# Optimization experiments

Measured on AMD Instinct MI355X. Metric: run time of the kernel, lower is better.

## Reference

```python
import jax, jax.numpy as jnp
import numpy as np

N = 50000          # nodes
E = 200000         # edges
IN_C = 16          # in_channels
HID_C = 32         # hidden_channels (NNConv output)
EDGE_D = 8         # edge_attr_dim
OUT_C = 32         # out_channels (gnn output)
MLP_H = 128        # q_head hidden_dim
N_ACT = 32         # num_actions


def setup_inputs() -> dict:
    key = jax.random.key(0)
    ks = jax.random.split(key, 16)
    s = 0.05
    inp = {
        "x": jax.random.normal(ks[0], (N, IN_C), jnp.float32),
        "edge_src": jax.random.randint(ks[1], (E,), 0, N, jnp.int32),
        "edge_dst": jax.random.randint(ks[2], (E,), 0, N, jnp.int32),
        "edge_attr": jax.random.normal(ks[3], (E, EDGE_D), jnp.float32),
        # edge_nn: Linear(EDGE_D, IN_C*HID_C) + ReLU
        "We": jax.random.normal(ks[4], (EDGE_D, IN_C * HID_C), jnp.float32) * s,
        "be": jnp.zeros((IN_C * HID_C,), jnp.float32),
        # NNConv root weight + bias
        "Wroot": jax.random.normal(ks[5], (IN_C, HID_C), jnp.float32) * s,
        "bconv": jnp.zeros((HID_C,), jnp.float32),
        # LayerNorm over hidden_channels
        "gamma": jnp.ones((HID_C,), jnp.float32),
        "beta": jnp.zeros((HID_C,), jnp.float32),
        # gnn.lin: Linear(HID_C, OUT_C)
        "Wlin": jax.random.normal(ks[6], (HID_C, OUT_C), jnp.float32) * s,
        "blin": jnp.zeros((OUT_C,), jnp.float32),
        # q_head: Linear(OUT_C, MLP_H) -> ReLU -> Linear(MLP_H, N_ACT)
        "Wq1": jax.random.normal(ks[7], (OUT_C, MLP_H), jnp.float32) * s,
        "bq1": jnp.zeros((MLP_H,), jnp.float32),
        "Wq2": jax.random.normal(ks[8], (MLP_H, N_ACT), jnp.float32) * s,
        "bq2": jnp.zeros((N_ACT,), jnp.float32),
    }
    return inp


def reference(x, edge_src, edge_dst, edge_attr,
              We, be, Wroot, bconv, gamma, beta,
              Wlin, blin, Wq1, bq1, Wq2, bq2):
    # --- NNConv: per-edge weight from edge MLP ---
    w_e = jax.nn.relu(edge_attr @ We + be)              # [E, IN_C*HID_C]
    w_e = w_e.reshape(E, IN_C, HID_C)
    x_j = x[edge_src]                                    # gather source feats [E, IN_C]
    msg = jnp.einsum('ei,eih->eh', x_j, w_e)             # per-edge matmul [E, HID_C]
    agg = jax.ops.segment_sum(msg, edge_dst, num_segments=N)  # scatter-add [N, HID_C]
    h = agg + x @ Wroot + bconv                          # root + bias
    # --- LayerNorm + ReLU + Linear ---
    mu = jnp.mean(h, axis=-1, keepdims=True)
    var = jnp.mean((h - mu) ** 2, axis=-1, keepdims=True)
    h = (h - mu) / jnp.sqrt(var + 1e-5) * gamma + beta
    h = jax.nn.relu(h)
    feat = h @ Wlin + blin                               # [N, OUT_C]
    # --- q_head MLP ---
    q = jax.nn.relu(feat @ Wq1 + bq1) @ Wq2 + bq2        # [N, N_ACT]
    return q.reshape(-1, N_ACT)
```

## Files before the change

kernel.cpp:

```cpp
#include <hip/hip_runtime.h>

#define NN   50000
#define NE   200000
#define INC  16
#define HIDC 32
#define EDGED 8
#define OUTC 32
#define MLPH 128
#define NACT 32

#define NPART 196

typedef float floatx4 __attribute__((ext_vector_type(4)));

__global__ __launch_bounds__(256) void hist_kernel(const int* __restrict__ edst,
                                                   int* __restrict__ deg) {
    int e = blockIdx.x * blockDim.x + threadIdx.x;
    if (e < NE) atomicAdd(&deg[edst[e]], 1);
}

__global__ __launch_bounds__(256) void partial_kernel(const int* __restrict__ deg,
                                                      int* __restrict__ partials) {
    __shared__ int sm[256];
    int t = threadIdx.x, i = blockIdx.x * 256 + t;
    sm[t] = (i < NN) ? deg[i] : 0;
    __syncthreads();
    #pragma unroll
    for (int off = 128; off > 0; off >>= 1) {
        if (t < off) sm[t] += sm[t + off];
        __syncthreads();
    }
    if (t == 0) partials[blockIdx.x] = sm[0];
}

__global__ __launch_bounds__(256) void scan_partials_kernel(const int* __restrict__ partials,
                                                            int* __restrict__ poff) {
    __shared__ int sm[256];
    int t = threadIdx.x;
    sm[t] = (t < NPART) ? partials[t] : 0;
    __syncthreads();
    for (int off = 1; off < 256; off <<= 1) {
        int v = (t >= off) ? sm[t - off] : 0;
        __syncthreads();
        sm[t] += v;
        __syncthreads();
    }
    poff[t] = (t == 0) ? 0 : sm[t - 1];
}

__global__ __launch_bounds__(256) void rowoff_kernel(const int* __restrict__ deg,
                                                     const int* __restrict__ poff,
                                                     int* __restrict__ row_off) {
    __shared__ int sm[256];
    int t = threadIdx.x, i = blockIdx.x * 256 + t;
    int d = (i < NN) ? deg[i] : 0;
    sm[t] = d;
    __syncthreads();
    for (int off = 1; off < 256; off <<= 1) {
        int v = (t >= off) ? sm[t - off] : 0;
        __syncthreads();
        sm[t] += v;
        __syncthreads();
    }
    int excl = sm[t] - d + poff[blockIdx.x];
    if (i < NN) {
        row_off[i] = excl;
        if (i == NN - 1) row_off[NN] = excl + d;
    }
}

__global__ __launch_bounds__(256) void build_pos_kernel(const int* __restrict__ edst,
                                                        const int* __restrict__ row_off,
                                                        int* __restrict__ cursor,
                                                        int* __restrict__ epos) {
    int e = blockIdx.x * blockDim.x + threadIdx.x;
    if (e < NE) {
        int dst = edst[e];
        epos[e] = row_off[dst] + atomicAdd(&cursor[dst], 1);
    }
}

__global__ __launch_bounds__(256, 2) void edge_q4_kernel(
    const float* __restrict__ x,
    const int*   __restrict__ esrc,
    const float* __restrict__ ea,
    const float* __restrict__ We,
    const float* __restrict__ be,
    const int*   __restrict__ epos,
    float*       __restrict__ sorted_msg)
{
    __shared__ float sWe2[4 * 1032];
    __shared__ float sbe2[4 * 132];
    int t = threadIdx.x;
    for (int idx = t; idx < 4 * 1032; idx += 256) {
        int l = idx / 1032, r = idx - l * 1032;
        float v = 0.f;
        if (r < 1024) {
            int d = r & 7, icc = r >> 3;
            int i = icc >> 3, cc = icc & 7;
            int h = ((cc & 4) << 2) + l * 4 + (cc & 3);
            v = We[d * 512 + i * 32 + h];
        }
        sWe2[idx] = v;
    }
    for (int idx = t; idx < 4 * 132; idx += 256) {
        int l = idx / 132, r = idx - l * 132;
        float v = 0.f;
        if (r < 128) {
            int i = r >> 3, cc = r & 7;
            int h = ((cc & 4) << 2) + l * 4 + (cc & 3);
            v = be[i * 32 + h];
        }
        sbe2[idx] = v;
    }
    __syncthreads();

    int q = blockIdx.x * 64 + (t >> 2);
    int l = t & 3;
    if (q >= NE / 4) return;

    int e0 = q, e1 = q + 50000, e2 = q + 100000, e3 = q + 150000;
    int s0 = esrc[e0], s1 = esrc[e1], s2 = esrc[e2], s3 = esrc[e3];
    int p0 = epos[e0], p1 = epos[e1], p2 = epos[e2], p3 = epos[e3];

    float ea0[8], ea1[8], ea2[8], ea3[8];
    {
        const float4* p;
        float4 a, b;
        p = reinterpret_cast<const float4*>(ea) + (size_t)e0 * 2; a = p[0]; b = p[1];
        ea0[0]=a.x; ea0[1]=a.y; ea0[2]=a.z; ea0[3]=a.w; ea0[4]=b.x; ea0[5]=b.y; ea0[6]=b.z; ea0[7]=b.w;
        p = reinterpret_cast<const float4*>(ea) + (size_t)e1 * 2; a = p[0]; b = p[1];
        ea1[0]=a.x; ea1[1]=a.y; ea1[2]=a.z; ea1[3]=a.w; ea1[4]=b.x; ea1[5]=b.y; ea1[6]=b.z; ea1[7]=b.w;
        p = reinterpret_cast<const float4*>(ea) + (size_t)e2 * 2; a = p[0]; b = p[1];
        ea2[0]=a.x; ea2[1]=a.y; ea2[2]=a.z; ea2[3]=a.w; ea2[4]=b.x; ea2[5]=b.y; ea2[6]=b.z; ea2[7]=b.w;
        p = reinterpret_cast<const float4*>(ea) + (size_t)e3 * 2; a = p[0]; b = p[1];
        ea3[0]=a.x; ea3[1]=a.y; ea3[2]=a.z; ea3[3]=a.w; ea3[4]=b.x; ea3[5]=b.y; ea3[6]=b.z; ea3[7]=b.w;
    }

    float m0[8], m1[8], m2[8], m3[8];
    #pragma unroll
    for (int c = 0; c < 8; ++c) { m0[c]=0.f; m1[c]=0.f; m2[c]=0.f; m3[c]=0.f; }

    const float* wl = sWe2 + l * 1032;
    const float* bl = sbe2 + l * 132;
    const float4* xp0 = reinterpret_cast<const float4*>(x) + (size_t)s0 * 4;
    const float4* xp1 = reinterpret_cast<const float4*>(x) + (size_t)s1 * 4;
    const float4* xp2 = reinterpret_cast<const float4*>(x) + (size_t)s2 * 4;
    const float4* xp3 = reinterpret_cast<const float4*>(x) + (size_t)s3 * 4;

    for (int i4 = 0; i4 < 4; ++i4) {
        float4 xv0 = xp0[i4], xv1 = xp1[i4], xv2 = xp2[i4], xv3 = xp3[i4];
        float xs0[4] = {xv0.x, xv0.y, xv0.z, xv0.w};
        float xs1[4] = {xv1.x, xv1.y, xv1.z, xv1.w};
        float xs2[4] = {xv2.x, xv2.y, xv2.z, xv2.w};
        float xs3[4] = {xv3.x, xv3.y, xv3.z, xv3.w};
        const float* wb4 = wl + i4 * 256;
        const float* bb4 = bl + i4 * 32;
        #pragma unroll
        for (int ii = 0; ii < 4; ++ii) {
            const float* wbase = wb4 + ii * 64;
            const float* bbase = bb4 + ii * 8;
            float xi0 = xs0[ii], xi1 = xs1[ii], xi2 = xs2[ii], xi3 = xs3[ii];
            #pragma unroll
            for (int cc = 0; cc < 8; ++cc) {
                const float* wr = wbase + cc * 8;
                float bv = bbase[cc];
                float w0 = bv, w1 = bv, w2 = bv, w3 = bv;
                #pragma unroll
                for (int d = 0; d < 8; ++d) {
                    float wd = wr[d];
                    w0 = fmaf(ea0[d], wd, w0);
                    w1 = fmaf(ea1[d], wd, w1);
                    w2 = fmaf(ea2[d], wd, w2);
                    w3 = fmaf(ea3[d], wd, w3);
                }
                w0 = fmaxf(w0, 0.f); w1 = fmaxf(w1, 0.f);
                w2 = fmaxf(w2, 0.f); w3 = fmaxf(w3, 0.f);
                m0[cc] = fmaf(xi0, w0, m0[cc]);
                m1[cc] = fmaf(xi1, w1, m1[cc]);
                m2[cc] = fmaf(xi2, w2, m2[cc]);
                m3[cc] = fmaf(xi3, w3, m3[cc]);
            }
        }
    }

    floatx4* o;
    floatx4 v;
    o = reinterpret_cast<floatx4*>(sorted_msg + (size_t)p0 * 32 + l * 4);
    v = (floatx4){m0[0], m0[1], m0[2], m0[3]}; __builtin_nontemporal_store(v, o);
    v = (floatx4){m0[4], m0[5], m0[6], m0[7]}; __builtin_nontemporal_store(v, o + 4);
    o = reinterpret_cast<floatx4*>(sorted_msg + (size_t)p1 * 32 + l * 4);
    v = (floatx4){m1[0], m1[1], m1[2], m1[3]}; __builtin_nontemporal_store(v, o);
    v = (floatx4){m1[4], m1[5], m1[6], m1[7]}; __builtin_nontemporal_store(v, o + 4);
    o = reinterpret_cast<floatx4*>(sorted_msg + (size_t)p2 * 32 + l * 4);
    v = (floatx4){m2[0], m2[1], m2[2], m2[3]}; __builtin_nontemporal_store(v, o);
    v = (floatx4){m2[4], m2[5], m2[6], m2[7]}; __builtin_nontemporal_store(v, o + 4);
    o = reinterpret_cast<floatx4*>(sorted_msg + (size_t)p3 * 32 + l * 4);
    v = (floatx4){m3[0], m3[1], m3[2], m3[3]}; __builtin_nontemporal_store(v, o);
    v = (floatx4){m3[4], m3[5], m3[6], m3[7]}; __builtin_nontemporal_store(v, o + 4);
}

__global__ __launch_bounds__(256, 2) void node_fused_kernel(
    const float* __restrict__ x,
    const float* __restrict__ sorted_msg,
    const int*   __restrict__ row_off,
    const float* __restrict__ Wroot,
    const float* __restrict__ bconv,
    const float* __restrict__ gamma,
    const float* __restrict__ beta,
    const float* __restrict__ Wlin,
    const float* __restrict__ blin,
    const float* __restrict__ Wq1,
    const float* __restrict__ bq1,
    const float* __restrict__ Wq2,
    const float* __restrict__ bq2,
    float* __restrict__ out)
{
    __shared__ float sw1[4 * 1032];
    int t = threadIdx.x;
    for (int w = t; w < 4096; w += 256) {
        int k = w >> 7, m = w & 127, l = m >> 5, j = m & 31;
        sw1[l * 1032 + k * 32 + j] = Wq1[w];
    }
    __syncthreads();

    int gid = blockIdx.x * 256 + t;
    int p = gid >> 2;
    int l = gid & 3;
    if (p >= NN / 2) return;
    int n0 = p * 2, n1 = p * 2 + 1;
    int o1 = l * 4;
    int o2 = 16 + l * 4;

    float h0[8], h1[8];
    {
        float4 a = *reinterpret_cast<const float4*>(bconv + o1);
        float4 b = *reinterpret_cast<const float4*>(bconv + o2);
        h0[0]=a.x; h0[1]=a.y; h0[2]=a.z; h0[3]=a.w;
        h0[4]=b.x; h0[5]=b.y; h0[6]=b.z; h0[7]=b.w;
        #pragma unroll
        for (int c = 0; c < 8; ++c) h1[c] = h0[c];
    }

    int r0 = row_off[n0], r1 = row_off[n1], r2 = row_off[n1 + 1];
    for (int k = r0; k < r1; ++k) {
        const float* row = sorted_msg + (size_t)k * 32;
        float4 a = *reinterpret_cast<const float4*>(row + o1);
        float4 b = *reinterpret_cast<const float4*>(row + o2);
        h0[0]+=a.x; h0[1]+=a.y; h0[2]+=a.z; h0[3]+=a.w;
        h0[4]+=b.x; h0[5]+=b.y; h0[6]+=b.z; h0[7]+=b.w;
    }
    for (int k = r1; k < r2; ++k) {
        const float* row = sorted_msg + (size_t)k * 32;
        float4 a = *reinterpret_cast<const float4*>(row + o1);
        float4 b = *reinterpret_cast<const float4*>(row + o2);
        h1[0]+=a.x; h1[1]+=a.y; h1[2]+=a.z; h1[3]+=a.w;
        h1[4]+=b.x; h1[5]+=b.y; h1[6]+=b.z; h1[7]+=b.w;
    }

    {
        const float4* xa = reinterpret_cast<const float4*>(x) + (size_t)n0 * 4;
        const float4* xb = reinterpret_cast<const float4*>(x) + (size_t)n1 * 4;
        #pragma unroll
        for (int i4 = 0; i4 < 4; ++i4) {
            float4 xv0 = xa[i4], xv1 = xb[i4];
            float xs0[4] = {xv0.x, xv0.y, xv0.z, xv0.w};
            float xs1[4] = {xv1.x, xv1.y, xv1.z, xv1.w};
            #pragma unroll
            for (int ii = 0; ii < 4; ++ii) {
                const float* wr = Wroot + (i4 * 4 + ii) * HIDC;
                float4 a = *reinterpret_cast<const float4*>(wr + o1);
                float4 b = *reinterpret_cast<const float4*>(wr + o2);
                float xi0 = xs0[ii], xi1 = xs1[ii];
                h0[0]=fmaf(xi0,a.x,h0[0]); h0[1]=fmaf(xi0,a.y,h0[1]);
                h0[2]=fmaf(xi0,a.z,h0[2]); h0[3]=fmaf(xi0,a.w,h0[3]);
                h0[4]=fmaf(xi0,b.x,h0[4]); h0[5]=fmaf(xi0,b.y,h0[5]);
                h0[6]=fmaf(xi0,b.z,h0[6]); h0[7]=fmaf(xi0,b.w,h0[7]);
                h1[0]=fmaf(xi1,a.x,h1[0]); h1[1]=fmaf(xi1,a.y,h1[1]);
                h1[2]=fmaf(xi1,a.z,h1[2]); h1[3]=fmaf(xi1,a.w,h1[3]);
                h1[4]=fmaf(xi1,b.x,h1[4]); h1[5]=fmaf(xi1,b.y,h1[5]);
                h1[6]=fmaf(xi1,b.z,h1[6]); h1[7]=fmaf(xi1,b.w,h1[7]);
            }
        }
    }

    float s0 = ((h0[0]+h0[1])+(h0[2]+h0[3])) + ((h0[4]+h0[5])+(h0[6]+h0[7]));
    float s1 = ((h1[0]+h1[1])+(h1[2]+h1[3])) + ((h1[4]+h1[5])+(h1[6]+h1[7]));
    s0 += __shfl_xor(s0, 1); s0 += __shfl_xor(s0, 2);
    s1 += __shfl_xor(s1, 1); s1 += __shfl_xor(s1, 2);
    float mu0 = s0 * (1.f / HIDC), mu1 = s1 * (1.f / HIDC);
    float v0 = 0.f, v1 = 0.f;
    #pragma unroll
    for (int c = 0; c < 8; ++c) {
        float d0 = h0[c] - mu0; v0 = fmaf(d0, d0, v0);
        float d1 = h1[c] - mu1; v1 = fmaf(d1, d1, v1);
    }
    v0 += __shfl_xor(v0, 1); v0 += __shfl_xor(v0, 2);
    v1 += __shfl_xor(v1, 1); v1 += __shfl_xor(v1, 2);
    float rs0 = rsqrtf(v0 * (1.f / HIDC) + 1e-5f);
    float rs1 = rsqrtf(v1 * (1.f / HIDC) + 1e-5f);
    {
        float4 g0 = *reinterpret_cast<const float4*>(gamma + o1);
        float4 g1 = *reinterpret_cast<const float4*>(gamma + o2);
        float4 b0 = *reinterpret_cast<const float4*>(beta + o1);
        float4 b1 = *reinterpret_cast<const float4*>(beta + o2);
        float gs[8] = {g0.x,g0.y,g0.z,g0.w,g1.x,g1.y,g1.z,g1.w};
        float bs[8] = {b0.x,b0.y,b0.z,b0.w,b1.x,b1.y,b1.z,b1.w};
        #pragma unroll
        for (int c = 0; c < 8; ++c) {
            h0[c] = fmaxf(fmaf((h0[c] - mu0) * rs0, gs[c], bs[c]), 0.f);
            h1[c] = fmaxf(fmaf((h1[c] - mu1) * rs1, gs[c], bs[c]), 0.f);
        }
    }

    float fA[8], fB[8];
    {
        float4 a = *reinterpret_cast<const float4*>(blin + o1);
        float4 b = *reinterpret_cast<const float4*>(blin + o2);
        fA[0]=a.x; fA[1]=a.y; fA[2]=a.z; fA[3]=a.w;
        fA[4]=b.x; fA[5]=b.y; fA[6]=b.z; fA[7]=b.w;
        #pragma unroll
        for (int c = 0; c < 8; ++c) fB[c] = fA[c];
    }
    #pragma unroll
    for (int srcl = 0; srcl < 4; ++srcl) {
        #pragma unroll
        for (int c = 0; c < 8; ++c) {
            float hv0 = __shfl(h0[c], srcl, 4);
            float hv1 = __shfl(h1[c], srcl, 4);
            int k = ((c & 4) << 2) + srcl * 4 + (c & 3);
            const float* wr = Wlin + k * OUTC;
            float4 a = *reinterpret_cast<const float4*>(wr + o1);
            float4 b = *reinterpret_cast<const float4*>(wr + o2);
            fA[0]=fmaf(hv0,a.x,fA[0]); fA[1]=fmaf(hv0,a.y,fA[1]);
            fA[2]=fmaf(hv0,a.z,fA[2]); fA[3]=fmaf(hv0,a.w,fA[3]);
            fA[4]=fmaf(hv0,b.x,fA[4]); fA[5]=fmaf(hv0,b.y,fA[5]);
            fA[6]=fmaf(hv0,b.z,fA[6]); fA[7]=fmaf(hv0,b.w,fA[7]);
            fB[0]=fmaf(hv1,a.x,fB[0]); fB[1]=fmaf(hv1,a.y,fB[1]);
            fB[2]=fmaf(hv1,a.z,fB[2]); fB[3]=fmaf(hv1,a.w,fB[3]);
            fB[4]=fmaf(hv1,b.x,fB[4]); fB[5]=fmaf(hv1,b.y,fB[5]);
            fB[6]=fmaf(hv1,b.z,fB[6]); fB[7]=fmaf(hv1,b.w,fB[7]);
        }
    }

    float f0[OUTC], f1[OUTC];
    #pragma unroll
    for (int srcl = 0; srcl < 4; ++srcl) {
        #pragma unroll
        for (int c = 0; c < 8; ++c) {
            int k = ((c & 4) << 2) + srcl * 4 + (c & 3);
            f0[k] = __shfl(fA[c], srcl, 4);
            f1[k] = __shfl(fB[c], srcl, 4);
        }
    }

    float acc0[32], acc1[32];
    {
        const float4* b4 = reinterpret_cast<const float4*>(bq1 + l * 32);
        #pragma unroll
        for (int j4 = 0; j4 < 8; ++j4) {
            float4 b = b4[j4];
            acc0[j4*4+0]=b.x; acc0[j4*4+1]=b.y; acc0[j4*4+2]=b.z; acc0[j4*4+3]=b.w;
            acc1[j4*4+0]=b.x; acc1[j4*4+1]=b.y; acc1[j4*4+2]=b.z; acc1[j4*4+3]=b.w;
        }
    }
    const float* w1 = sw1 + l * 1032;
    #pragma unroll
    for (int k = 0; k < 32; ++k) {
        float fk0 = f0[k], fk1 = f1[k];
        const float* wr = w1 + k * 32;
        #pragma unroll
        for (int j = 0; j < 32; ++j) {
            float wj = wr[j];
            acc0[j] = fmaf(fk0, wj, acc0[j]);
            acc1[j] = fmaf(fk1, wj, acc1[j]);
        }
    }
    #pragma unroll
    for (int j = 0; j < 32; ++j) {
        acc0[j] = fmaxf(acc0[j], 0.f);
        acc1[j] = fmaxf(acc1[j], 0.f);
    }

    float q0[8], q1[8];
    {
        const float4* b4 = reinterpret_cast<const float4*>(bq2 + l * 8);
        float4 a = b4[0], b = b4[1];
        q0[0]=a.x; q0[1]=a.y; q0[2]=a.z; q0[3]=a.w;
        q0[4]=b.x; q0[5]=b.y; q0[6]=b.z; q0[7]=b.w;
        #pragma unroll
        for (int c = 0; c < 8; ++c) q1[c] = q0[c];
    }
    #pragma unroll
    for (int srcl = 0; srcl < 4; ++srcl) {
        #pragma unroll
        for (int j = 0; j < 32; ++j) {
            float a0 = __shfl(acc0[j], srcl, 4);
            float a1 = __shfl(acc1[j], srcl, 4);
            int m = srcl * 32 + j;
            const float4* w2 = reinterpret_cast<const float4*>(Wq2 + m * NACT + l * 8);
            float4 wa = w2[0], wb = w2[1];
            q0[0]=fmaf(a0,wa.x,q0[0]); q0[1]=fmaf(a0,wa.y,q0[1]);
            q0[2]=fmaf(a0,wa.z,q0[2]); q0[3]=fmaf(a0,wa.w,q0[3]);
            q0[4]=fmaf(a0,wb.x,q0[4]); q0[5]=fmaf(a0,wb.y,q0[5]);
            q0[6]=fmaf(a0,wb.z,q0[6]); q0[7]=fmaf(a0,wb.w,q0[7]);
            q1[0]=fmaf(a1,wa.x,q1[0]); q1[1]=fmaf(a1,wa.y,q1[1]);
            q1[2]=fmaf(a1,wa.z,q1[2]); q1[3]=fmaf(a1,wa.w,q1[3]);
            q1[4]=fmaf(a1,wb.x,q1[4]); q1[5]=fmaf(a1,wb.y,q1[5]);
            q1[6]=fmaf(a1,wb.z,q1[6]); q1[7]=fmaf(a1,wb.w,q1[7]);
        }
    }

    float4* o;
    o = reinterpret_cast<float4*>(out + (size_t)n0 * NACT + l * 8);
    o[0] = make_float4(q0[0], q0[1], q0[2], q0[3]);
    o[1] = make_float4(q0[4], q0[5], q0[6], q0[7]);
    o = reinterpret_cast<float4*>(out + (size_t)n1 * NACT + l * 8);
    o[0] = make_float4(q1[0], q1[1], q1[2], q1[3]);
    o[1] = make_float4(q1[4], q1[5], q1[6], q1[7]);
}

extern "C" void kernel_launch(void* const* d_in, const int* in_sizes, int n_in,
                              void* d_out, int out_size, void* d_ws, size_t ws_size,
                              hipStream_t stream) {
    const float* x     = (const float*)d_in[0];
    const int*   esrc  = (const int*)d_in[1];
    const int*   edst  = (const int*)d_in[2];
    const float* ea    = (const float*)d_in[3];
    const float* We    = (const float*)d_in[4];
    const float* be    = (const float*)d_in[5];
    const float* Wroot = (const float*)d_in[6];
    const float* bconv = (const float*)d_in[7];
    const float* gamma = (const float*)d_in[8];
    const float* beta  = (const float*)d_in[9];
    const float* Wlin  = (const float*)d_in[10];
    const float* blin  = (const float*)d_in[11];
    const float* Wq1   = (const float*)d_in[12];
    const float* bq1   = (const float*)d_in[13];
    const float* Wq2   = (const float*)d_in[14];
    const float* bq2   = (const float*)d_in[15];
    float* out = (float*)d_out;

    char* ws = (char*)d_ws;
    int*   deg        = (int*)(ws + 0);
    int*   cursor     = (int*)(ws + 200704);
    int*   row_off    = (int*)(ws + 401408);
    int*   partials   = (int*)(ws + 603136);
    int*   poff       = (int*)(ws + 604160);
    int*   epos       = (int*)(ws + 605184);
    float* sorted_msg = (float*)(ws + 1405952);

    hipMemsetAsync(deg, 0, 2 * 200704, stream);

    hist_kernel<<<(NE + 255) / 256, 256, 0, stream>>>(edst, deg);
    partial_kernel<<<NPART, 256, 0, stream>>>(deg, partials);
    scan_partials_kernel<<<1, 256, 0, stream>>>(partials, poff);
    rowoff_kernel<<<NPART, 256, 0, stream>>>(deg, poff, row_off);
    build_pos_kernel<<<(NE + 255) / 256, 256, 0, stream>>>(edst, row_off, cursor, epos);
    edge_q4_kernel<<<(NE / 4 + 63) / 64, 256, 0, stream>>>(x, esrc, ea, We, be,
                                                           epos, sorted_msg);
    node_fused_kernel<<<(NN / 2 * 4 + 255) / 256, 256, 0, stream>>>(
        x, sorted_msg, row_off, Wroot, bconv, gamma, beta,
        Wlin, blin, Wq1, bq1, Wq2, bq2, out);
}
```

Before: 126.7 us.

## Merge CSR build kernels and halve edges per thread in edge kernel

The histogram kernel now records each edge's atomic slot, so the separate build_pos pass and its cursor array go away. The partial-sum scan is folded into the row-offset kernel, with each block summing the preceding partials serially. The edge kernel now handles two edges per thread group instead of four, fully unrolls over input channels, and raises the occupancy hint from 2 to 4 blocks. This cuts two kernel launches and one atomic pass, but adds a serial prefix loop per block and more weight re-reads from shared memory per edge.

```diff
diff --git a/kernel.cpp b/kernel.cpp
--- a/kernel.cpp
+++ b/kernel.cpp
@@ -13,10 +13,11 @@
 
 typedef float floatx4 __attribute__((ext_vector_type(4)));
 
-__global__ __launch_bounds__(256) void hist_kernel(const int* __restrict__ edst,
-                                                   int* __restrict__ deg) {
+__global__ __launch_bounds__(256) void hist_slot_kernel(const int* __restrict__ edst,
+                                                        int* __restrict__ deg,
+                                                        int* __restrict__ slot) {
     int e = blockIdx.x * blockDim.x + threadIdx.x;
-    if (e < NE) atomicAdd(&deg[edst[e]], 1);
+    if (e < NE) slot[e] = atomicAdd(&deg[edst[e]], 1);
 }
 
 __global__ __launch_bounds__(256) void partial_kernel(const int* __restrict__ deg,
@@ -33,26 +34,18 @@
     if (t == 0) partials[blockIdx.x] = sm[0];
 }
 
-__global__ __launch_bounds__(256) void scan_partials_kernel(const int* __restrict__ partials,
-                                                            int* __restrict__ poff) {
+__global__ __launch_bounds__(256) void rowoff2_kernel(const int* __restrict__ deg,
+                                                      const int* __restrict__ partials,
+                                                      int* __restrict__ row_off) {
+    __shared__ int sp[NPART];
     __shared__ int sm[256];
-    int t = threadIdx.x;
-    sm[t] = (t < NPART) ? partials[t] : 0;
+    int t = threadIdx.x, bid = blockIdx.x;
+    if (t < NPART) sp[t] = partials[t];
     __syncthreads();
-    for (int off = 1; off < 256; off <<= 1) {
-        int v = (t >= off) ? sm[t - off] : 0;
-        __syncthreads();
-        sm[t] += v;
-        __syncthreads();
-    }
-    poff[t] = (t == 0) ? 0 : sm[t - 1];
-}
-
-__global__ __launch_bounds__(256) void rowoff_kernel(const int* __restrict__ deg,
-                                                     const int* __restrict__ poff,
-                                                     int* __restrict__ row_off) {
-    __shared__ int sm[256];
-    int t = threadIdx.x, i = blockIdx.x * 256 + t;
+    int base = 0;
+    for (int i = 0; i < bid; ++i) base += sp[i];
+
+    int i = bid * 256 + t;
     int d = (i < NN) ? deg[i] : 0;
     sm[t] = d;
     __syncthreads();
@@ -62,31 +55,22 @@
         sm[t] += v;
         __syncthreads();
     }
-    int excl = sm[t] - d + poff[blockIdx.x];
+    int excl = sm[t] - d + base;
     if (i < NN) {
         row_off[i] = excl;
         if (i == NN - 1) row_off[NN] = excl + d;
     }
 }
 
-__global__ __launch_bounds__(256) void build_pos_kernel(const int* __restrict__ edst,
-                                                        const int* __restrict__ row_off,
-                                                        int* __restrict__ cursor,
-                                                        int* __restrict__ epos) {
-    int e = blockIdx.x * blockDim.x + threadIdx.x;
-    if (e < NE) {
-        int dst = edst[e];
-        epos[e] = row_off[dst] + atomicAdd(&cursor[dst], 1);
-    }
-}
-
-__global__ __launch_bounds__(256, 2) void edge_q4_kernel(
+__global__ __launch_bounds__(256, 4) void edge_q2u_kernel(
     const float* __restrict__ x,
     const int*   __restrict__ esrc,
+    const int*   __restrict__ edst,
     const float* __restrict__ ea,
     const float* __restrict__ We,
     const float* __restrict__ be,
-    const int*   __restrict__ epos,
+    const int*   __restrict__ row_off,
+    const int*   __restrict__ slot,
     float*       __restrict__ sorted_msg)
 {
     __shared__ float sWe2[4 * 1032];
@@ -117,13 +101,14 @@
 
     int q = blockIdx.x * 64 + (t >> 2);
     int l = t & 3;
-    if (q >= NE / 4) return;
-
-    int e0 = q, e1 = q + 50000, e2 = q + 100000, e3 = q + 150000;
-    int s0 = esrc[e0], s1 = esrc[e1], s2 = esrc[e2], s3 = esrc[e3];
-    int p0 = epos[e0], p1 = epos[e1], p2 = epos[e2], p3 = epos[e3];
-
-    float ea0[8], ea1[8], ea2[8], ea3[8];
+    if (q >= NE / 2) return;
+
+    int e0 = q, e1 = q + 100000;
+    int s0 = esrc[e0], s1 = esrc[e1];
+    int p0 = row_off[edst[e0]] + slot[e0];
+    int p1 = row_off[edst[e1]] + slot[e1];
+
+    float ea0[8], ea1[8];
     {
         const float4* p;
         float4 a, b;
@@ -131,56 +116,46 @@
         ea0[0]=a.x; ea0[1]=a.y; ea0[2]=a.z; ea0[3]=a.w; ea0[4]=b.x; ea0[5]=b.y; ea0[6]=b.z; ea0[7]=b.w;
         p = reinterpret_cast<const float4*>(ea) + (size_t)e1 * 2; a = p[0]; b = p[1];
         ea1[0]=a.x; ea1[1]=a.y; ea1[2]=a.z; ea1[3]=a.w; ea1[4]=b.x; ea1[5]=b.y; ea1[6]=b.z; ea1[7]=b.w;
-        p = reinterpret_cast<const float4*>(ea) + (size_t)e2 * 2; a = p[0]; b = p[1];
-        ea2[0]=a.x; ea2[1]=a.y; ea2[2]=a.z; ea2[3]=a.w; ea2[4]=b.x; ea2[5]=b.y; ea2[6]=b.z; ea2[7]=b.w;
-        p = reinterpret_cast<const float4*>(ea) + (size_t)e3 * 2; a = p[0]; b = p[1];
-        ea3[0]=a.x; ea3[1]=a.y; ea3[2]=a.z; ea3[3]=a.w; ea3[4]=b.x; ea3[5]=b.y; ea3[6]=b.z; ea3[7]=b.w;
-    }
-
-    float m0[8], m1[8], m2[8], m3[8];
-    #pragma unroll
-    for (int c = 0; c < 8; ++c) { m0[c]=0.f; m1[c]=0.f; m2[c]=0.f; m3[c]=0.f; }
+    }
+
+    float xs0[16], xs1[16];
+    {
+        const float4* xp0 = reinterpret_cast<const float4*>(x) + (size_t)s0 * 4;
+        const float4* xp1 = reinterpret_cast<const float4*>(x) + (size_t)s1 * 4;
+        #pragma unroll
+        for (int i4 = 0; i4 < 4; ++i4) {
+            float4 v0 = xp0[i4], v1 = xp1[i4];
+            xs0[i4*4+0]=v0.x; xs0[i4*4+1]=v0.y; xs0[i4*4+2]=v0.z; xs0[i4*4+3]=v0.w;
+            xs1[i4*4+0]=v1.x; xs1[i4*4+1]=v1.y; xs1[i4*4+2]=v1.z; xs1[i4*4+3]=v1.w;
+        }
+    }
+
+    float m0[8], m1[8];
+    #pragma unroll
+    for (int c = 0; c < 8; ++c) { m0[c]=0.f; m1[c]=0.f; }
 
     const float* wl = sWe2 + l * 1032;
     const float* bl = sbe2 + l * 132;
-    const float4* xp0 = reinterpret_cast<const float4*>(x) + (size_t)s0 * 4;
-    const float4* xp1 = reinterpret_cast<const float4*>(x) + (size_t)s1 * 4;
-    const float4* xp2 = reinterpret_cast<const float4*>(x) + (size_t)s2 * 4;
-    const float4* xp3 = reinterpret_cast<const float4*>(x) + (size_t)s3 * 4;
-
-    for (int i4 = 0; i4 < 4; ++i4) {
-        float4 xv0 = xp0[i4], xv1 = xp1[i4], xv2 = xp2[i4], xv3 = xp3[i4];
-        float xs0[4] = {xv0.x, xv0.y, xv0.z, xv0.w};
-        float xs1[4] = {xv1.x, xv1.y, xv1.z, xv1.w};
-        float xs2[4] = {xv2.x, xv2.y, xv2.z, xv2.w};
-        float xs3[4] = {xv3.x, xv3.y, xv3.z, xv3.w};
-        const float* wb4 = wl + i4 * 256;
-        const float* bb4 = bl + i4 * 32;
-        #pragma unroll
-        for (int ii = 0; ii < 4; ++ii) {
-            const float* wbase = wb4 + ii * 64;
-            const float* bbase = bb4 + ii * 8;
-            float xi0 = xs0[ii], xi1 = xs1[ii], xi2 = xs2[ii], xi3 = xs3[ii];
+
+    #pragma unroll
+    for (int i = 0; i < 16; ++i) {
+        const float* wbase = wl + i * 64;
+        const float* bbase = bl + i * 8;
+        float xi0 = xs0[i], xi1 = xs1[i];
+        #pragma unroll
+        for (int cc = 0; cc < 8; ++cc) {
+            const float* wr = wbase + cc * 8;
+            float bv = bbase[cc];
+            float w0 = bv, w1 = bv;
             #pragma unroll
-            for (int cc = 0; cc < 8; ++cc) {
-                const float* wr = wbase + cc * 8;
-                float bv = bbase[cc];
-                float w0 = bv, w1 = bv, w2 = bv, w3 = bv;
-                #pragma unroll
-                for (int d = 0; d < 8; ++d) {
-                    float wd = wr[d];
-                    w0 = fmaf(ea0[d], wd, w0);
-                    w1 = fmaf(ea1[d], wd, w1);
-                    w2 = fmaf(ea2[d], wd, w2);
-                    w3 = fmaf(ea3[d], wd, w3);
-                }
-                w0 = fmaxf(w0, 0.f); w1 = fmaxf(w1, 0.f);
-                w2 = fmaxf(w2, 0.f); w3 = fmaxf(w3, 0.f);
-                m0[cc] = fmaf(xi0, w0, m0[cc]);
-                m1[cc] = fmaf(xi1, w1, m1[cc]);
-                m2[cc] = fmaf(xi2, w2, m2[cc]);
-                m3[cc] = fmaf(xi3, w3, m3[cc]);
+            for (int d = 0; d < 8; ++d) {
+                float wd = wr[d];
+                w0 = fmaf(ea0[d], wd, w0);
+                w1 = fmaf(ea1[d], wd, w1);
             }
+            w0 = fmaxf(w0, 0.f); w1 = fmaxf(w1, 0.f);
+            m0[cc] = fmaf(xi0, w0, m0[cc]);
+            m1[cc] = fmaf(xi1, w1, m1[cc]);
         }
     }
 
@@ -192,12 +167,6 @@
     o = reinterpret_cast<floatx4*>(sorted_msg + (size_t)p1 * 32 + l * 4);
     v = (floatx4){m1[0], m1[1], m1[2], m1[3]}; __builtin_nontemporal_store(v, o);
     v = (floatx4){m1[4], m1[5], m1[6], m1[7]}; __builtin_nontemporal_store(v, o + 4);
-    o = reinterpret_cast<floatx4*>(sorted_msg + (size_t)p2 * 32 + l * 4);
-    v = (floatx4){m2[0], m2[1], m2[2], m2[3]}; __builtin_nontemporal_store(v, o);
-    v = (floatx4){m2[4], m2[5], m2[6], m2[7]}; __builtin_nontemporal_store(v, o + 4);
-    o = reinterpret_cast<floatx4*>(sorted_msg + (size_t)p3 * 32 + l * 4);
-    v = (floatx4){m3[0], m3[1], m3[2], m3[3]}; __builtin_nontemporal_store(v, o);
-    v = (floatx4){m3[4], m3[5], m3[6], m3[7]}; __builtin_nontemporal_store(v, o + 4);
 }
 
 __global__ __launch_bounds__(256, 2) void node_fused_kernel(
@@ -443,22 +412,18 @@
 
     char* ws = (char*)d_ws;
     int*   deg        = (int*)(ws + 0);
-    int*   cursor     = (int*)(ws + 200704);
-    int*   row_off    = (int*)(ws + 401408);
-    int*   partials   = (int*)(ws + 603136);
-    int*   poff       = (int*)(ws + 604160);
-    int*   epos       = (int*)(ws + 605184);
-    float* sorted_msg = (float*)(ws + 1405952);
-
-    hipMemsetAsync(deg, 0, 2 * 200704, stream);
-
-    hist_kernel<<<(NE + 255) / 256, 256, 0, stream>>>(edst, deg);
+    int*   slot       = (int*)(ws + 200704);
+    int*   row_off    = (int*)(ws + 1001472);
+    int*   partials   = (int*)(ws + 1203200);
+    float* sorted_msg = (float*)(ws + 1204224);
+
+    hipMemsetAsync(deg, 0, 200704, stream);
+
+    hist_slot_kernel<<<(NE + 255) / 256, 256, 0, stream>>>(edst, deg, slot);
     partial_kernel<<<NPART, 256, 0, stream>>>(deg, partials);
-    scan_partials_kernel<<<1, 256, 0, stream>>>(partials, poff);
-    rowoff_kernel<<<NPART, 256, 0, stream>>>(deg, poff, row_off);
-    build_pos_kernel<<<(NE + 255) / 256, 256, 0, stream>>>(edst, row_off, cursor, epos);
-    edge_q4_kernel<<<(NE / 4 + 63) / 64, 256, 0, stream>>>(x, esrc, ea, We, be,
-                                                           epos, sorted_msg);
+    rowoff2_kernel<<<NPART, 256, 0, stream>>>(deg, partials, row_off);
+    edge_q2u_kernel<<<(NE / 2 * 4 + 255) / 256, 256, 0, stream>>>(
+        x, esrc, edst, ea, We, be, row_off, slot, sorted_msg);
     node_fused_kernel<<<(NN / 2 * 4 + 255) / 256, 256, 0, stream>>>(
         x, sorted_msg, row_off, Wroot, bconv, gamma, beta,
         Wlin, blin, Wq1, bq1, Wq2, bq2, out);
```

Result: slower. 302.3 us (+138.6%).
